# Kernel optimization log

Hardware: AMD Instinct MI355X
Metric: run time of the kernel (lower is better)

Reference implementation:

```python
import jax, jax.numpy as jnp
import numpy as np

B, S, E = 8192, 100, 64
H1, H2 = 128, 64


def setup_inputs() -> dict:
    key = jax.random.key(0)
    ks = jax.random.split(key, 9)
    query = jax.random.normal(ks[0], (B, E), dtype=jnp.float32)
    keys = jax.random.normal(ks[1], (B, S, E), dtype=jnp.float32)
    # valid history lengths in [1, S] (at least 1 so softmax row is finite)
    keys_length = jnp.maximum(jax.random.randint(ks[2], (B,), 0, S), 1).astype(jnp.int32)
    s = 0.05
    W0 = jax.random.normal(ks[3], (4 * E, H1), dtype=jnp.float32) * s
    b0 = jnp.zeros((H1,), dtype=jnp.float32)
    W1 = jax.random.normal(ks[4], (H1, H2), dtype=jnp.float32) * s
    b1 = jnp.zeros((H2,), dtype=jnp.float32)
    W2 = jax.random.normal(ks[5], (H2, 1), dtype=jnp.float32) * s
    b2 = jnp.zeros((1,), dtype=jnp.float32)
    return {"query": query, "keys": keys, "keys_length": keys_length,
            "W0": W0, "b0": b0, "W1": W1, "b1": b1, "W2": W2, "b2": b2}


def reference(query, keys, keys_length, W0, b0, W1, b1, W2, b2):
    # query: [B,E] -> broadcast to [B,S,E]
    q = jnp.broadcast_to(query[:, None, :], keys.shape)
    feats = jnp.concatenate([q, keys, q * keys, q - keys], axis=-1)  # [B,S,4E]
    h = jax.nn.relu(jnp.einsum('bsf,fh->bsh', feats, W0) + b0)  # dropout is inference no-op
    h = jax.nn.relu(jnp.einsum('bsf,fh->bsh', h, W1) + b1)
    scores = (jnp.einsum('bsf,fo->bso', h, W2) + b2)[..., 0]  # [B,S]
    mask = jnp.arange(keys.shape[1])[None, :] < keys_length[:, None]  # [B,S]
    scores = jnp.where(mask, scores, -jnp.inf)
    attn = jax.nn.softmax(scores, axis=1)  # [B,S]
    out = jnp.einsum('bs,bse->be', attn, keys)  # [B,E]
    return out, attn
```

## Files before the change

kernel.cpp:

```cpp
#include <hip/hip_runtime.h>
#include <math.h>


#define B_TOT 8192
#define SEQ 100
#define EDIM 64
#define H1D 128
#define H2D 64

__global__ __launch_bounds__(256, 2)
void din_fused(const float* __restrict__ query,
               const float* __restrict__ keys,
               const int* __restrict__ klen,
               const float* __restrict__ W0,
               const float* __restrict__ b0,
               const float* __restrict__ W1,
               const float* __restrict__ b1,
               const float* __restrict__ W2,
               const float* __restrict__ b2,
               float* __restrict__ out,
               float* __restrict__ attn)
{
    const int b = blockIdx.x;
    const int t = threadIdx.x;
    const int lane = t & 63;
    const int wave = t >> 6;

    __shared__ float q_lds[EDIM];
    __shared__ float A_h[H1D];
    __shared__ float MT[H1D][65];
    __shared__ float keys_tile[16][EDIM];
    __shared__ float h0t[16][H1D];
    __shared__ float part[16 * 256];
    __shared__ float scores[112];
    __shared__ float red[256];

    const int len = klen[b];
    const float* qrow = query + (size_t)b * EDIM;
    const float* krow = keys + (size_t)b * SEQ * EDIM;

    if (t < EDIM) q_lds[t] = qrow[t];
    __syncthreads();

    const int j  = t & 63;
    const int hb = t >> 6;
    float w1r[32];
#pragma unroll
    for (int i = 0; i < 32; ++i)
        w1r[i] = W1[(hb * 32 + i) * H2D + j];
    const float b1r = b1[j];
    const float w2r = W2[j];
    const float b2r = b2[0];

    if (t < H1D) {
        float acc = b0[t];
        for (int e = 0; e < EDIM; ++e)
            acc += q_lds[e] * (W0[e * H1D + t] + W0[(192 + e) * H1D + t]);
        A_h[t] = acc;
    }
    {
        const int h = t & 127;
        const int ebase = t >> 7;
#pragma unroll
        for (int i = 0; i < 32; ++i) {
            int e = i * 2 + ebase;
            float v = W0[(64 + e) * H1D + h] - W0[(192 + e) * H1D + h]
                    + q_lds[e] * W0[(128 + e) * H1D + h];
            MT[h][e] = v;
        }
    }
    __syncthreads();

    for (int st = 0; st < 7; ++st) {
        const int s0 = st * 16;
        {
            int row = s0 + (t >> 4);
            int col = (t & 15) * 4;
            float4 k4 = make_float4(0.f, 0.f, 0.f, 0.f);
            if (row < SEQ)
                k4 = *reinterpret_cast<const float4*>(krow + row * EDIM + col);
            *reinterpret_cast<float4*>(&keys_tile[t >> 4][col]) = k4;
        }
        __syncthreads();

        {
            const int h  = t & 127;
            const int sg = (t >> 7) * 8;
            float acc[8];
            const float a0 = A_h[h];
#pragma unroll
            for (int si = 0; si < 8; ++si) acc[si] = a0;
            for (int e4 = 0; e4 < EDIM; e4 += 4) {
                float m0 = MT[h][e4], m1 = MT[h][e4 + 1],
                      m2 = MT[h][e4 + 2], m3 = MT[h][e4 + 3];
#pragma unroll
                for (int si = 0; si < 8; ++si) {
                    float4 k = *reinterpret_cast<const float4*>(&keys_tile[sg + si][e4]);
                    acc[si] = fmaf(m0, k.x, acc[si]);
                    acc[si] = fmaf(m1, k.y, acc[si]);
                    acc[si] = fmaf(m2, k.z, acc[si]);
                    acc[si] = fmaf(m3, k.w, acc[si]);
                }
            }
#pragma unroll
            for (int si = 0; si < 8; ++si)
                h0t[sg + si][h] = fmaxf(acc[si], 0.f);
        }
        __syncthreads();

        for (int s = 0; s < 16; ++s) {
            float acc = 0.f;
#pragma unroll
            for (int i4 = 0; i4 < 32; i4 += 4) {
                float4 hv = *reinterpret_cast<const float4*>(&h0t[s][hb * 32 + i4]);
                acc = fmaf(hv.x, w1r[i4],     acc);
                acc = fmaf(hv.y, w1r[i4 + 1], acc);
                acc = fmaf(hv.z, w1r[i4 + 2], acc);
                acc = fmaf(hv.w, w1r[i4 + 3], acc);
            }
            part[s * 256 + t] = acc;
        }
        __syncthreads();

#pragma unroll
        for (int pass = 0; pass < 4; ++pass) {
            int s = pass * 4 + wave;
            float v = b1r + part[s * 256 + j] + part[s * 256 + 64 + j]
                    + part[s * 256 + 128 + j] + part[s * 256 + 192 + j];
            v = fmaxf(v, 0.f);
            float sc = v * w2r;
#pragma unroll
            for (int off = 32; off; off >>= 1)
                sc += __shfl_xor(sc, off, 64);
            if (lane == 0) scores[s0 + s] = sc + b2r;
        }
        __syncthreads();
    }

    if (wave == 0) {
        float v0 = (lane < len) ? scores[lane] : -INFINITY;
        int s1 = lane + 64;
        float v1 = (s1 < len) ? scores[s1] : -INFINITY;
        float m = fmaxf(v0, v1);
#pragma unroll
        for (int off = 32; off; off >>= 1)
            m = fmaxf(m, __shfl_xor(m, off, 64));
        float e0 = (lane < len) ? expf(v0 - m) : 0.f;
        float e1 = (s1 < len) ? expf(v1 - m) : 0.f;
        float ssum = e0 + e1;
#pragma unroll
        for (int off = 32; off; off >>= 1)
            ssum += __shfl_xor(ssum, off, 64);
        float inv = 1.f / ssum;
        scores[lane] = e0 * inv;
        if (s1 < 112) scores[s1] = e1 * inv;
    }
    __syncthreads();

    if (t < SEQ) attn[(size_t)b * SEQ + t] = scores[t];

    {
        float acc = 0.f;
        const int e = j;
        for (int s = wave * 25; s < wave * 25 + 25; ++s)
            acc = fmaf(scores[s], krow[s * EDIM + e], acc);
        red[t] = acc;
    }
    __syncthreads();
    if (t < EDIM)
        out[(size_t)b * EDIM + t] = red[t] + red[64 + t] + red[128 + t] + red[192 + t];
}

extern "C" void kernel_launch(void* const* d_in, const int* in_sizes, int n_in,
                              void* d_out, int out_size, void* d_ws, size_t ws_size,
                              hipStream_t stream)
{
    const float* query = (const float*)d_in[0];
    const float* keys  = (const float*)d_in[1];
    const int*   klen  = (const int*)d_in[2];
    const float* W0 = (const float*)d_in[3];
    const float* b0 = (const float*)d_in[4];
    const float* W1 = (const float*)d_in[5];
    const float* b1 = (const float*)d_in[6];
    const float* W2 = (const float*)d_in[7];
    const float* b2 = (const float*)d_in[8];

    float* out  = (float*)d_out;
    float* attn = out + (size_t)B_TOT * EDIM;

    din_fused<<<dim3(B_TOT), dim3(256), 0, stream>>>(
        query, keys, klen, W0, b0, W1, b1, W2, b2, out, attn);
}
```

Measured before the change: 1.050 ms.

## Register-block both MLP layers over 56-row sequence tiles and fold softmax into output

Processes the sequence in two 56-row tiles instead of seven 16-row tiles. Each thread now computes a 7x4 block of the first layer and a 7x2 block of the second layer from LDS, which gives more reuse per LDS read. The second layer's partial-sum buffer and its extra reduction pass are replaced by a 32-lane shuffle reduction. Softmax no longer subtracts the row max: it stores exp(score), accumulates the attention-weighted keys from the keys tile already in LDS instead of re-reading global memory, and normalises once at the end. The costs are a larger LDS footprint, W1 read from global/cache inside the loop, and possible overflow because the max is not subtracted.

```diff
diff --git a/kernel.cpp b/kernel.cpp
--- a/kernel.cpp
+++ b/kernel.cpp
@@ -7,6 +7,10 @@
 #define EDIM 64
 #define H1D 128
 #define H2D 64
+#define STILE 56
+#define KPAD 68
+
+#define F4C(v, i) ((i) == 0 ? (v).x : ((i) == 1 ? (v).y : ((i) == 2 ? (v).z : (v).w)))
 
 __global__ __launch_bounds__(256, 2)
 void din_fused(const float* __restrict__ query,
@@ -23,152 +27,165 @@
 {
     const int b = blockIdx.x;
     const int t = threadIdx.x;
-    const int lane = t & 63;
-    const int wave = t >> 6;
-
-    __shared__ float q_lds[EDIM];
-    __shared__ float A_h[H1D];
-    __shared__ float MT[H1D][65];
-    __shared__ float keys_tile[16][EDIM];
-    __shared__ float h0t[16][H1D];
-    __shared__ float part[16 * 256];
-    __shared__ float scores[112];
+
+    __shared__ float M_lds[64 * 128];
+    __shared__ float keys_t[STILE * KPAD];
+    __shared__ float h0[STILE * 128];
+    __shared__ float A_lds[128];
+    __shared__ float q_lds[64];
+    __shared__ float p_all[112];
     __shared__ float red[256];
+    __shared__ float l_sh;
 
     const int len = klen[b];
     const float* qrow = query + (size_t)b * EDIM;
     const float* krow = keys + (size_t)b * SEQ * EDIM;
 
-    if (t < EDIM) q_lds[t] = qrow[t];
-    __syncthreads();
-
-    const int j  = t & 63;
-    const int hb = t >> 6;
-    float w1r[32];
-#pragma unroll
-    for (int i = 0; i < 32; ++i)
-        w1r[i] = W1[(hb * 32 + i) * H2D + j];
-    const float b1r = b1[j];
-    const float w2r = W2[j];
-    const float b2r = b2[0];
-
-    if (t < H1D) {
-        float acc = b0[t];
-        for (int e = 0; e < EDIM; ++e)
-            acc += q_lds[e] * (W0[e * H1D + t] + W0[(192 + e) * H1D + t]);
-        A_h[t] = acc;
-    }
+    if (t < 64) q_lds[t] = qrow[t];
+    __syncthreads();
+
     {
-        const int h = t & 127;
-        const int ebase = t >> 7;
+        const int h = t & 127, eb = t >> 7;
 #pragma unroll
         for (int i = 0; i < 32; ++i) {
-            int e = i * 2 + ebase;
-            float v = W0[(64 + e) * H1D + h] - W0[(192 + e) * H1D + h]
-                    + q_lds[e] * W0[(128 + e) * H1D + h];
-            MT[h][e] = v;
-        }
-    }
-    __syncthreads();
-
-    for (int st = 0; st < 7; ++st) {
-        const int s0 = st * 16;
+            int e = i * 2 + eb;
+            M_lds[e * 128 + h] = W0[(64 + e) * 128 + h] - W0[(192 + e) * 128 + h]
+                               + q_lds[e] * W0[(128 + e) * 128 + h];
+        }
+    }
+    if (t < 128) {
+        float a = b0[t];
+        for (int e = 0; e < 64; ++e)
+            a += q_lds[e] * (W0[e * 128 + t] + W0[(192 + e) * 128 + t]);
+        A_lds[t] = a;
+    }
+
+    const int jx = t & 31;
+    const int syg = t >> 5;
+    const float b1a = b1[jx * 2], b1b = b1[jx * 2 + 1];
+    const float w2a = W2[jx * 2], w2b = W2[jx * 2 + 1];
+    const float b2v = b2[0];
+    float out_acc = 0.f;
+    __syncthreads();
+
+    for (int tile = 0; tile < 2; ++tile) {
+        const int s0 = tile * STILE;
+
+#pragma unroll
+        for (int i = 0; i < 4; ++i) {
+            int idx = i * 256 + t;
+            if (idx < STILE * 16) {
+                int r = idx >> 4, c = (idx & 15) * 4;
+                int gs = s0 + r;
+                float4 v = make_float4(0.f, 0.f, 0.f, 0.f);
+                if (gs < SEQ) v = *reinterpret_cast<const float4*>(krow + gs * 64 + c);
+                *reinterpret_cast<float4*>(&keys_t[r * KPAD + c]) = v;
+            }
+        }
+        __syncthreads();
+
         {
-            int row = s0 + (t >> 4);
-            int col = (t & 15) * 4;
-            float4 k4 = make_float4(0.f, 0.f, 0.f, 0.f);
-            if (row < SEQ)
-                k4 = *reinterpret_cast<const float4*>(krow + row * EDIM + col);
-            *reinterpret_cast<float4*>(&keys_tile[t >> 4][col]) = k4;
+            float acc[7][4];
+            float4 a4 = *reinterpret_cast<float4*>(&A_lds[jx * 4]);
+#pragma unroll
+            for (int si = 0; si < 7; ++si) {
+                acc[si][0] = a4.x; acc[si][1] = a4.y; acc[si][2] = a4.z; acc[si][3] = a4.w;
+            }
+#pragma unroll 2
+            for (int ec = 0; ec < 16; ++ec) {
+                float4 kc[7], mm[4];
+#pragma unroll
+                for (int si = 0; si < 7; ++si)
+                    kc[si] = *reinterpret_cast<float4*>(&keys_t[(syg * 7 + si) * KPAD + ec * 4]);
+#pragma unroll
+                for (int ei = 0; ei < 4; ++ei)
+                    mm[ei] = *reinterpret_cast<float4*>(&M_lds[(ec * 4 + ei) * 128 + jx * 4]);
+#pragma unroll
+                for (int ei = 0; ei < 4; ++ei) {
+#pragma unroll
+                    for (int si = 0; si < 7; ++si) {
+                        float k = F4C(kc[si], ei);
+                        acc[si][0] = fmaf(k, mm[ei].x, acc[si][0]);
+                        acc[si][1] = fmaf(k, mm[ei].y, acc[si][1]);
+                        acc[si][2] = fmaf(k, mm[ei].z, acc[si][2]);
+                        acc[si][3] = fmaf(k, mm[ei].w, acc[si][3]);
+                    }
+                }
+            }
+#pragma unroll
+            for (int si = 0; si < 7; ++si) {
+                float4 r;
+                r.x = fmaxf(acc[si][0], 0.f); r.y = fmaxf(acc[si][1], 0.f);
+                r.z = fmaxf(acc[si][2], 0.f); r.w = fmaxf(acc[si][3], 0.f);
+                *reinterpret_cast<float4*>(&h0[(syg * 7 + si) * 128 + jx * 4]) = r;
+            }
         }
         __syncthreads();
 
         {
-            const int h  = t & 127;
-            const int sg = (t >> 7) * 8;
-            float acc[8];
-            const float a0 = A_h[h];
-#pragma unroll
-            for (int si = 0; si < 8; ++si) acc[si] = a0;
-            for (int e4 = 0; e4 < EDIM; e4 += 4) {
-                float m0 = MT[h][e4], m1 = MT[h][e4 + 1],
-                      m2 = MT[h][e4 + 2], m3 = MT[h][e4 + 3];
-#pragma unroll
-                for (int si = 0; si < 8; ++si) {
-                    float4 k = *reinterpret_cast<const float4*>(&keys_tile[sg + si][e4]);
-                    acc[si] = fmaf(m0, k.x, acc[si]);
-                    acc[si] = fmaf(m1, k.y, acc[si]);
-                    acc[si] = fmaf(m2, k.z, acc[si]);
-                    acc[si] = fmaf(m3, k.w, acc[si]);
+            float acc2[7][2];
+#pragma unroll
+            for (int si = 0; si < 7; ++si) { acc2[si][0] = 0.f; acc2[si][1] = 0.f; }
+#pragma unroll 4
+            for (int hc = 0; hc < 32; ++hc) {
+                float4 hv[7];
+#pragma unroll
+                for (int si = 0; si < 7; ++si)
+                    hv[si] = *reinterpret_cast<float4*>(&h0[(syg * 7 + si) * 128 + hc * 4]);
+                float2 w[4];
+#pragma unroll
+                for (int i = 0; i < 4; ++i)
+                    w[i] = *reinterpret_cast<const float2*>(&W1[(hc * 4 + i) * 64 + jx * 2]);
+#pragma unroll
+                for (int i = 0; i < 4; ++i) {
+#pragma unroll
+                    for (int si = 0; si < 7; ++si) {
+                        float hvv = F4C(hv[si], i);
+                        acc2[si][0] = fmaf(hvv, w[i].x, acc2[si][0]);
+                        acc2[si][1] = fmaf(hvv, w[i].y, acc2[si][1]);
+                    }
                 }
             }
 #pragma unroll
-            for (int si = 0; si < 8; ++si)
-                h0t[sg + si][h] = fmaxf(acc[si], 0.f);
-        }
-        __syncthreads();
-
-        for (int s = 0; s < 16; ++s) {
-            float acc = 0.f;
-#pragma unroll
-            for (int i4 = 0; i4 < 32; i4 += 4) {
-                float4 hv = *reinterpret_cast<const float4*>(&h0t[s][hb * 32 + i4]);
-                acc = fmaf(hv.x, w1r[i4],     acc);
-                acc = fmaf(hv.y, w1r[i4 + 1], acc);
-                acc = fmaf(hv.z, w1r[i4 + 2], acc);
-                acc = fmaf(hv.w, w1r[i4 + 3], acc);
-            }
-            part[s * 256 + t] = acc;
-        }
-        __syncthreads();
-
-#pragma unroll
-        for (int pass = 0; pass < 4; ++pass) {
-            int s = pass * 4 + wave;
-            float v = b1r + part[s * 256 + j] + part[s * 256 + 64 + j]
-                    + part[s * 256 + 128 + j] + part[s * 256 + 192 + j];
-            v = fmaxf(v, 0.f);
-            float sc = v * w2r;
-#pragma unroll
-            for (int off = 32; off; off >>= 1)
-                sc += __shfl_xor(sc, off, 64);
-            if (lane == 0) scores[s0 + s] = sc + b2r;
-        }
-        __syncthreads();
-    }
-
-    if (wave == 0) {
-        float v0 = (lane < len) ? scores[lane] : -INFINITY;
-        int s1 = lane + 64;
-        float v1 = (s1 < len) ? scores[s1] : -INFINITY;
-        float m = fmaxf(v0, v1);
-#pragma unroll
-        for (int off = 32; off; off >>= 1)
-            m = fmaxf(m, __shfl_xor(m, off, 64));
-        float e0 = (lane < len) ? expf(v0 - m) : 0.f;
-        float e1 = (s1 < len) ? expf(v1 - m) : 0.f;
-        float ssum = e0 + e1;
-#pragma unroll
-        for (int off = 32; off; off >>= 1)
-            ssum += __shfl_xor(ssum, off, 64);
-        float inv = 1.f / ssum;
-        scores[lane] = e0 * inv;
-        if (s1 < 112) scores[s1] = e1 * inv;
-    }
-    __syncthreads();
-
-    if (t < SEQ) attn[(size_t)b * SEQ + t] = scores[t];
-
-    {
-        float acc = 0.f;
-        const int e = j;
-        for (int s = wave * 25; s < wave * 25 + 25; ++s)
-            acc = fmaf(scores[s], krow[s * EDIM + e], acc);
-        red[t] = acc;
-    }
-    __syncthreads();
-    if (t < EDIM)
-        out[(size_t)b * EDIM + t] = red[t] + red[64 + t] + red[128 + t] + red[192 + t];
+            for (int si = 0; si < 7; ++si) {
+                float v = fmaxf(acc2[si][0] + b1a, 0.f) * w2a
+                        + fmaxf(acc2[si][1] + b1b, 0.f) * w2b;
+#pragma unroll
+                for (int off = 1; off < 32; off <<= 1)
+                    v += __shfl_xor(v, off, 64);
+                int gs = s0 + syg * 7 + si;
+                if (jx == 0)
+                    p_all[gs] = (gs < len) ? expf(v + b2v) : 0.f;
+            }
+        }
+        __syncthreads();
+
+        {
+            const int e = t & 63, sg = t >> 6;
+#pragma unroll
+            for (int si = 0; si < 14; ++si) {
+                int sl = sg * 14 + si;
+                out_acc = fmaf(p_all[s0 + sl], keys_t[sl * KPAD + e], out_acc);
+            }
+        }
+        __syncthreads();
+    }
+
+    red[t] = out_acc;
+    __syncthreads();
+    if (t < 64) {
+        float v = p_all[t] + (t < 48 ? p_all[64 + t] : 0.f);
+#pragma unroll
+        for (int off = 1; off < 64; off <<= 1)
+            v += __shfl_xor(v, off, 64);
+        if (t == 0) l_sh = v;
+    }
+    __syncthreads();
+    const float linv = 1.f / l_sh;
+    if (t < 64)
+        out[(size_t)b * 64 + t] = (red[t] + red[64 + t] + red[128 + t] + red[192 + t]) * linv;
+    if (t < 100)
+        attn[(size_t)b * 100 + t] = p_all[t] * linv;
 }
 
 extern "C" void kernel_launch(void* const* d_in, const int* in_sizes, int n_in,
```

Result: faster. 868.1 us (-17.3%).
